# Kernel tuning notes

Measured on AMD Instinct MI355X. Metric: run time of the kernel, lower is better.

The kernel has to match this reference:

```python
import jax, jax.numpy as jnp
import numpy as np

IN_FEATURES = 1024
N_CLASSES = 50257
CUTOFFS = [2000, 10000]      # head covers [0,2000); clusters [2000,10000), [10000,50257)
DIV_VALUE = 4.0
IGNORE_INDEX = -1
N_ROWS = 4096
HEAD_SIZE = CUTOFFS[0] + len(CUTOFFS)  # 2002 (head classes + one slot per tail cluster)
HSZ = [int(IN_FEATURES // (DIV_VALUE ** (i + 1))) for i in range(len(CUTOFFS))]  # [256, 64]
BOUNDS = CUTOFFS + [N_CLASSES]


def setup_inputs() -> dict:
    key = jax.random.key(0)
    ks = jax.random.split(key, 8)
    x = jax.random.normal(ks[0], (N_ROWS, IN_FEATURES), dtype=jnp.float32)
    target = jax.random.randint(ks[1], (N_ROWS,), 0, N_CLASSES, dtype=jnp.int64)
    drop = jax.random.uniform(ks[2], (N_ROWS,)) < 0.1
    target = jnp.where(drop, IGNORE_INDEX, target)
    s = 1.0 / np.sqrt(IN_FEATURES)
    head_w = jax.random.normal(ks[3], (HEAD_SIZE, IN_FEATURES), dtype=jnp.float32) * s
    proj0 = jax.random.normal(ks[4], (HSZ[0], IN_FEATURES), dtype=jnp.float32) * s
    out0 = jax.random.normal(ks[5], (BOUNDS[1] - BOUNDS[0], HSZ[0]), dtype=jnp.float32) * (1.0 / np.sqrt(HSZ[0]))
    proj1 = jax.random.normal(ks[6], (HSZ[1], IN_FEATURES), dtype=jnp.float32) * s
    out1 = jax.random.normal(ks[7], (BOUNDS[2] - BOUNDS[1], HSZ[1]), dtype=jnp.float32) * (1.0 / np.sqrt(HSZ[1]))
    return {"x": x, "target": target, "head_w": head_w,
            "proj0": proj0, "out0": out0, "proj1": proj1, "out1": out1}


def reference(x, target, head_w, proj0, out0, proj1, out1):
    # head: [N, cutoff0 + n_clusters] logits, shared log-softmax
    head_lp = jax.nn.log_softmax(jnp.einsum('nd,hd->nh', x, head_w), axis=-1)
    rows = jnp.arange(x.shape[0])
    valid = target != IGNORE_INDEX
    t = jnp.where(valid, target, 0)

    # head-band targets: log prob directly from head
    t_head = jnp.clip(t, 0, CUTOFFS[0] - 1)
    logp = head_lp[rows, t_head]

    # tail clusters: head cluster-slot logprob + within-cluster logprob
    tails = [(proj0, out0), (proj1, out1)]
    for i, (proj, out) in enumerate(tails):
        low, high = BOUNDS[i], BOUNDS[i + 1]
        # [N, hsz] @ [hsz, osz] -> [N, osz] cluster logits
        cl_lp = jax.nn.log_softmax(
            jnp.einsum('nh,oh->no', jnp.einsum('nd,hd->nh', x, proj), out), axis=-1)
        rel = jnp.clip(t - low, 0, high - low - 1)
        cand = head_lp[:, CUTOFFS[0] + i] + cl_lp[rows, rel]
        logp = jnp.where((t >= low) & (t < high), cand, logp)

    # ignore-index filter + mean == masked mean over valid rows
    vf = valid.astype(logp.dtype)
    loss = -(logp * vf).sum() / vf.sum()
    return loss
```

## Files before the change

kernel.cpp:

```cpp
#include <hip/hip_runtime.h>
#include <hip/hip_bf16.h>

typedef __attribute__((ext_vector_type(8))) short bf16x8;
typedef __attribute__((ext_vector_type(4))) float f32x4;
typedef unsigned short u16;

constexpr int NR      = 4096;
constexpr int INF     = 1024;
constexpr int HEAD_N  = 2002;
constexpr int HEAD_NP = 2048;
constexpr int C0_LO   = 2000, C0_HI = 10000;
constexpr int C0_N    = 8000;
constexpr int C1_N    = 40257;
constexpr int C1_NP   = 40320;
constexpr int K0      = 256;
constexpr int K1      = 64;
constexpr int PCAT    = 320;
constexpr int PCAT_P  = 384;
constexpr int WCAT_R  = HEAD_NP + PCAT_P;
constexpr int IGNORE  = -1;
constexpr float LOG2E = 1.4426950408889634f;
constexpr float LN2   = 0.6931471805599453f;

constexpr int S0      = 16;
constexpr int S1      = 10;
constexpr int NHP     = 32;
constexpr int MEGA_GRID = 1024 + 512;

static __device__ __forceinline__ u16 f32_to_bf16(float f) {
    unsigned int u = __float_as_uint(f);
    return (u16)((u + 0x7FFFu + ((u >> 16) & 1u)) >> 16);
}

static __device__ __forceinline__ float fast_exp2(float x) {
#if __has_builtin(__builtin_amdgcn_exp2f)
    return __builtin_amdgcn_exp2f(x);
#else
    return __expf(x * LN2);
#endif
}

static __device__ __forceinline__ void gload_lds16(const u16* g, u16* l) {
    __builtin_amdgcn_global_load_lds(
        (const __attribute__((address_space(1))) unsigned int*)g,
        (__attribute__((address_space(3))) unsigned int*)l, 16, 0, 0);
}

struct CvtSegs { const float* s[6]; u16* d[6]; int n8[6]; float sc[6]; };

__global__ void cvt_multi(CvtSegs segs) {
    const int stride = gridDim.x * blockDim.x;
    const int gid = blockIdx.x * blockDim.x + threadIdx.x;
#pragma unroll
    for (int seg = 0; seg < 6; ++seg) {
        const float4* sp = (const float4*)segs.s[seg];
        bf16x8* dp = (bf16x8*)segs.d[seg];
        const int n8 = segs.n8[seg];
        const float sc = segs.sc[seg];
        for (int i = gid; i < n8; i += stride) {
            float4 a = sp[2 * i], b = sp[2 * i + 1];
            bf16x8 o;
            o[0] = (short)f32_to_bf16(a.x * sc); o[1] = (short)f32_to_bf16(a.y * sc);
            o[2] = (short)f32_to_bf16(a.z * sc); o[3] = (short)f32_to_bf16(a.w * sc);
            o[4] = (short)f32_to_bf16(b.x * sc); o[5] = (short)f32_to_bf16(b.y * sc);
            o[6] = (short)f32_to_bf16(b.z * sc); o[7] = (short)f32_to_bf16(b.w * sc);
            dp[i] = o;
        }
    }
}

__global__ void compact_kernel(const int* __restrict__ tgt,
                               int* __restrict__ c0list, int* __restrict__ c1list,
                               int* __restrict__ crow, int* __restrict__ cnts) {
    __shared__ int b0, b1;
    if (threadIdx.x == 0) { b0 = 0; b1 = 0; }
    __syncthreads();
#pragma unroll
    for (int i = 0; i < 4; ++i) {
        const int r = threadIdx.x + i * 1024;
        const int t = tgt[r];
        if (t >= C0_LO && t < C0_HI) { int s = atomicAdd(&b0, 1); c0list[s] = r; crow[r] = s; }
        else if (t >= C0_HI)         { int s = atomicAdd(&b1, 1); c1list[s] = r; crow[r] = s; }
        else crow[r] = 0;
    }
    __syncthreads();
    const int c0 = b0, c1 = b1;
    const int p0 = (c0 + 127) & ~127, p1 = (c1 + 127) & ~127;
    if (threadIdx.x == 0) { cnts[0] = c0; cnts[1] = c1; cnts[2] = p0; cnts[3] = p1; }
    for (int i = c0 + (int)threadIdx.x; i < p0; i += 1024) c0list[i] = 0;
    for (int i = c1 + (int)threadIdx.x; i < p1; i += 1024) c1list[i] = 0;
}

__launch_bounds__(256, 2)
__global__ void proj_tile(const u16* __restrict__ A, const u16* __restrict__ B,
                          float* __restrict__ HF, u16* __restrict__ HB)
{
    constexpr int K = INF;
    __shared__ u16 ldsA[128 * 64];
    __shared__ u16 ldsB[128 * 64];
    const int tid = threadIdx.x, wid = tid >> 6, lane = tid & 63;
    const int wr = wid >> 1, wc = wid & 1;
    const int row0 = blockIdx.x * 128, col0 = blockIdx.y * 128;

    f32x4 acc[4][4];
#pragma unroll
    for (int m = 0; m < 4; ++m)
#pragma unroll
        for (int n = 0; n < 4; ++n) acc[m][n] = (f32x4){0.f, 0.f, 0.f, 0.f};

    const int srow = lane >> 3;
    const int ssw  = (lane & 7) ^ srow;

    for (int ks = 0; ks < K / 64; ++ks) {
        const int k0 = ks * 64;
#pragma unroll
        for (int q = 0; q < 4; ++q) {
            const int c = q * 4 + wid, row = c * 8 + srow;
            gload_lds16(A + (size_t)(row0 + row) * K + k0 + ssw * 8, ldsA + c * 512);
        }
#pragma unroll
        for (int q = 0; q < 4; ++q) {
            const int c = q * 4 + wid, row = c * 8 + srow;
            gload_lds16(B + (size_t)(col0 + row) * K + k0 + ssw * 8, ldsB + c * 512);
        }
        __syncthreads();
        const bf16x8* A8 = (const bf16x8*)ldsA;
        const bf16x8* B8 = (const bf16x8*)ldsB;
        bf16x8 af[4][2], bfr[4][2];
#pragma unroll
        for (int m = 0; m < 4; ++m) {
            const int ar = wr * 64 + m * 16 + (lane & 15);
#pragma unroll
            for (int ks2 = 0; ks2 < 2; ++ks2)
                af[m][ks2] = A8[ar * 8 + ((ks2 * 4 + (lane >> 4)) ^ (ar & 7))];
        }
#pragma unroll
        for (int n = 0; n < 4; ++n) {
            const int br = wc * 64 + n * 16 + (lane & 15);
#pragma unroll
            for (int ks2 = 0; ks2 < 2; ++ks2)
                bfr[n][ks2] = B8[br * 8 + ((ks2 * 4 + (lane >> 4)) ^ (br & 7))];
        }
#pragma unroll
        for (int ks2 = 0; ks2 < 2; ++ks2)
#pragma unroll
            for (int m = 0; m < 4; ++m)
#pragma unroll
                for (int n = 0; n < 4; ++n)
                    acc[m][n] = __builtin_amdgcn_mfma_f32_16x16x32_bf16(
                        af[m][ks2], bfr[n][ks2], acc[m][n], 0, 0, 0);
        __syncthreads();
    }
#pragma unroll
    for (int m = 0; m < 4; ++m)
#pragma unroll
        for (int n = 0; n < 4; ++n) {
            const int col = col0 + wc * 64 + n * 16 + (lane & 15);
            if (col < PCAT) {
#pragma unroll
                for (int r = 0; r < 4; ++r) {
                    const int row = row0 + wr * 64 + m * 16 + (lane >> 4) * 4 + r;
                    const float v = acc[m][n][r];
                    HF[(size_t)row * PCAT + col] = v;
                    HB[(size_t)row * PCAT + col] = f32_to_bf16(v);
                }
            }
        }
}

static __device__ void head_section(int rb, int ct,
                                    const u16* __restrict__ A, const u16* __restrict__ B,
                                    const int* __restrict__ tgt,
                                    float* __restrict__ SEHp, float* __restrict__ TL,
                                    u16* ldsA, u16* ldsB, int* sth)
{
    constexpr int K = INF;
    const int tid = threadIdx.x, wid = tid >> 6, lane = tid & 63;
    const int wr = wid >> 1, wc = wid & 1;
    const int row0 = rb * 128, col0 = ct * 128;

    if (tid < 128) {
        int t = tgt[row0 + tid];
        sth[tid] = (t < 0) ? 0 : (t < C0_LO ? t : (t < C0_HI ? C0_LO : C0_LO + 1));
    }

    f32x4 acc[4][4];
#pragma unroll
    for (int m = 0; m < 4; ++m)
#pragma unroll
        for (int n = 0; n < 4; ++n) acc[m][n] = (f32x4){0.f, 0.f, 0.f, 0.f};

    const int srow = lane >> 3;
    const int ssw  = (lane & 7) ^ srow;

    for (int ks = 0; ks < K / 64; ++ks) {
        const int k0 = ks * 64;
#pragma unroll
        for (int q = 0; q < 4; ++q) {
            const int c = q * 4 + wid, row = c * 8 + srow;
            gload_lds16(A + (size_t)(row0 + row) * K + k0 + ssw * 8, ldsA + c * 512);
        }
#pragma unroll
        for (int q = 0; q < 4; ++q) {
            const int c = q * 4 + wid, row = c * 8 + srow;
            gload_lds16(B + (size_t)(col0 + row) * K + k0 + ssw * 8, ldsB + c * 512);
        }
        __syncthreads();
        const bf16x8* A8 = (const bf16x8*)ldsA;
        const bf16x8* B8 = (const bf16x8*)ldsB;
        bf16x8 af[4][2], bfr[4][2];
#pragma unroll
        for (int m = 0; m < 4; ++m) {
            const int ar = wr * 64 + m * 16 + (lane & 15);
#pragma unroll
            for (int ks2 = 0; ks2 < 2; ++ks2)
                af[m][ks2] = A8[ar * 8 + ((ks2 * 4 + (lane >> 4)) ^ (ar & 7))];
        }
#pragma unroll
        for (int n = 0; n < 4; ++n) {
            const int br = wc * 64 + n * 16 + (lane & 15);
#pragma unroll
            for (int ks2 = 0; ks2 < 2; ++ks2)
                bfr[n][ks2] = B8[br * 8 + ((ks2 * 4 + (lane >> 4)) ^ (br & 7))];
        }
#pragma unroll
        for (int ks2 = 0; ks2 < 2; ++ks2)
#pragma unroll
            for (int m = 0; m < 4; ++m)
#pragma unroll
                for (int n = 0; n < 4; ++n)
                    acc[m][n] = __builtin_amdgcn_mfma_f32_16x16x32_bf16(
                        af[m][ks2], bfr[n][ks2], acc[m][n], 0, 0, 0);
        __syncthreads();
    }

    const int slot = ct * 2 + wc;
#pragma unroll
    for (int m = 0; m < 4; ++m) {
        f32x4 rs = (f32x4){0.f, 0.f, 0.f, 0.f};
#pragma unroll
        for (int n = 0; n < 4; ++n) {
            const int cls = col0 + wc * 64 + n * 16 + (lane & 15);
            if (cls < HEAD_N) {
#pragma unroll
                for (int r = 0; r < 4; ++r) {
                    rs[r] += fast_exp2(acc[m][n][r]);
                    const int lrow = wr * 64 + m * 16 + (lane >> 4) * 4 + r;
                    if (sth[lrow] == cls) TL[row0 + lrow] = acc[m][n][r];
                }
            }
        }
#pragma unroll
        for (int msk = 1; msk < 16; msk <<= 1)
#pragma unroll
            for (int r = 0; r < 4; ++r) rs[r] += __shfl_xor(rs[r], msk, 64);
        if ((lane & 15) == 0) {
            const int rbase = row0 + wr * 64 + m * 16 + (lane >> 4) * 4;
#pragma unroll
            for (int r = 0; r < 4; ++r) SEHp[(size_t)slot * NR + rbase + r] = rs[r];
        }
    }
}

template<int K, int CT>
static __device__ void sumexp_section(const u16* __restrict__ Hbase, int ldh,
                                      const int* __restrict__ list,
                                      const u16* __restrict__ W,
                                      int nreal, int ntiles, int tps,
                                      int rb, int split, float* __restrict__ SEp,
                                      u16* lds)
{
    constexpr int MSETS = 2;
    constexpr int NKF   = K / 32;
    constexpr int SLOTS = K / 8;
    constexpr int CHUNKS = CT * K * 2 / 4096;
    constexpr int RPC   = 256 / SLOTS;
    constexpr int NT    = CT / 16;

    const int tid = threadIdx.x, wid = tid >> 6, lane = tid & 63;
    const int row0 = rb * 128 + wid * 32;

    const int t0 = split * tps;
    const int t1 = min(t0 + tps, ntiles);

    bf16x8 afr[MSETS][NKF];
#pragma unroll
    for (int m = 0; m < MSETS; ++m) {
        const int orow = list[row0 + m * 16 + (lane & 15)];
        const u16* hr = Hbase + (size_t)orow * ldh + (lane >> 4) * 8;
#pragma unroll
        for (int kf = 0; kf < NKF; ++kf)
            afr[m][kf] = *(const bf16x8*)(hr + kf * 32);
    }

    float rs[MSETS][4];
#pragma unroll
    for (int m = 0; m < MSETS; ++m)
#pragma unroll
        for (int r = 0; r < 4; ++r) rs[m][r] = 0.f;

    const int trow  = tid / SLOTS;
    const int swoff = ((tid % SLOTS) ^ (trow & 7)) * 8;

    auto STAGE = [&](int t, int buf) {
        const u16* wb = W + (size_t)t * CT * K + (size_t)trow * K + swoff;
        u16* lb = lds + buf * (CT * K) + wid * 512;
#pragma unroll
        for (int c = 0; c < CHUNKS; ++c)
            gload_lds16(wb + (size_t)c * RPC * K, lb + c * 2048);
    };

    int cur = 0;
    STAGE(t0, 0);
    __syncthreads();

    for (int t = t0; t < t1; ++t) {
        if (t + 1 < t1) STAGE(t + 1, cur ^ 1);
        const bf16x8* B8 = (const bf16x8*)(lds + cur * (CT * K));
        const bool full = (t + 1) * CT <= nreal;
#pragma unroll
        for (int n = 0; n < NT; ++n) {
            const int br = n * 16 + (lane & 15);
            bf16x8 bfr[NKF];
#pragma unroll
            for (int kf = 0; kf < NKF; ++kf)
                bfr[kf] = B8[br * SLOTS + ((kf * 4 + (lane >> 4)) ^ (br & 7))];
            f32x4 acc[MSETS];
#pragma unroll
            for (int m = 0; m < MSETS; ++m) acc[m] = (f32x4){0.f, 0.f, 0.f, 0.f};
#pragma unroll
            for (int m = 0; m < MSETS; ++m)
#pragma unroll
                for (int kf = 0; kf < NKF; ++kf)
                    acc[m] = __builtin_amdgcn_mfma_f32_16x16x32_bf16(
                        afr[m][kf], bfr[kf], acc[m], 0, 0, 0);
            if (full || (t * CT + n * 16 + (lane & 15)) < nreal) {
#pragma unroll
                for (int m = 0; m < MSETS; ++m)
#pragma unroll
                    for (int r = 0; r < 4; ++r) rs[m][r] += fast_exp2(acc[m][r]);
            }
        }
        __syncthreads();
        cur ^= 1;
    }

#pragma unroll
    for (int msk = 1; msk < 16; msk <<= 1)
#pragma unroll
        for (int m = 0; m < MSETS; ++m)
#pragma unroll
            for (int r = 0; r < 4; ++r) rs[m][r] += __shfl_xor(rs[m][r], msk, 64);
    if ((lane & 15) == 0) {
        const int rbase = row0 + (lane >> 4) * 4;
#pragma unroll
        for (int m = 0; m < MSETS; ++m)
#pragma unroll
            for (int r = 0; r < 4; ++r)
                SEp[(size_t)split * NR + rbase + m * 16 + r] = rs[m][r];
    }
}

__launch_bounds__(256, 3)
__global__ void mega_kernel(const u16* __restrict__ xb, const u16* __restrict__ wcatb,
                            const u16* __restrict__ hcatb,
                            const u16* __restrict__ o0b, const u16* __restrict__ o1b,
                            const int* __restrict__ tgt,
                            const int* __restrict__ c0list, const int* __restrict__ c1list,
                            const int* __restrict__ cnts,
                            float* __restrict__ SEHp, float* __restrict__ TL,
                            float* __restrict__ C0p, float* __restrict__ C1p)
{
    __shared__ u16 smem[2][8192];
    __shared__ int sth[128];
    const int bid = blockIdx.x;

    if (bid < 1024) {
        if ((bid & 1) == 0) {
            const int h = bid >> 1;
            head_section(h >> 4, h & 15, xb, wcatb, tgt, SEHp, TL,
                         smem[0], smem[1], sth);
        } else {
            const int c = bid >> 1;
            const int rb = c / S1, split = c - rb * S1;
            if (rb * 128 < cnts[3])
                sumexp_section<K1, 128>(hcatb + 256, PCAT, c1list, o1b,
                                        C1_N, C1_NP / 128, 32, rb, split, C1p, smem[0]);
        }
    } else {
        const int idx = bid - 1024;
        const int rb = idx >> 4, split = idx & 15;
        if (rb * 128 < cnts[2])
            sumexp_section<K0, 32>(hcatb, PCAT, c0list, o0b,
                                   C0_N, C0_N / 32, 16, rb, split, C0p, smem[0]);
    }
}

__global__ void epilogue_kernel(const int* __restrict__ tgt, const float* __restrict__ tl,
                                const float* __restrict__ out0, const float* __restrict__ out1,
                                const float* __restrict__ hcatf,
                                const float* __restrict__ SEHp, const float* __restrict__ C0p,
                                const float* __restrict__ C1p, const int* __restrict__ crow,
                                float* __restrict__ rowlogp, float* __restrict__ rowvalid) {
    const int wid = threadIdx.x >> 6, lane = threadIdx.x & 63;
    const int r = blockIdx.x * 4 + wid;
    const int t = tgt[r];
    const bool valid = (t != IGNORE);
    const int tc = valid ? t : 0;
    const int band = (tc < C0_LO) ? 0 : (tc < C0_HI) ? 1 : 2;
    const int cr = crow[r];

    float p2 = 0.f;
    if (band == 1) {
        const float* hr = hcatf + (size_t)r * PCAT;
        const float* crp = out0 + (size_t)(tc - C0_LO) * K0;
        for (int k = lane; k < K0; k += 64) p2 += hr[k] * crp[k];
    } else if (band == 2) {
        p2 = hcatf[(size_t)r * PCAT + 256 + lane] * out1[(size_t)(tc - C0_HI) * K1 + lane];
    }
#pragma unroll
    for (int msk = 32; msk >= 1; msk >>= 1) p2 += __shfl_xor(p2, msk, 64);

    float hp = (lane < NHP) ? SEHp[(size_t)lane * NR + r] : 0.f;
    float cp = 0.f;
    if (band == 1 && lane < S0) cp = C0p[(size_t)lane * NR + cr];
    if (band == 2 && lane < S1) cp = C1p[(size_t)lane * NR + cr];
#pragma unroll
    for (int msk = 1; msk < 32; msk <<= 1) {
        hp += __shfl_xor(hp, msk, 64);
        cp += __shfl_xor(cp, msk, 64);
    }

    if (lane == 0) {
        float logp = LN2 * tl[r] - __logf(hp);
        if (band != 0) logp += p2 - __logf(cp);
        rowlogp[r]  = valid ? logp : 0.f;
        rowvalid[r] = valid ? 1.f : 0.f;
    }
}

__global__ void final_reduce(const float* __restrict__ rowlogp,
                             const float* __restrict__ rowvalid, float* __restrict__ out) {
    __shared__ float sl[256], sv[256];
    const int tid = threadIdx.x;
    float a = 0.f, b = 0.f;
    for (int i = tid; i < NR; i += 256) { a += rowlogp[i]; b += rowvalid[i]; }
    sl[tid] = a; sv[tid] = b;
    __syncthreads();
    for (int s = 128; s > 0; s >>= 1) {
        if (tid < s) { sl[tid] += sl[tid + s]; sv[tid] += sv[tid + s]; }
        __syncthreads();
    }
    if (tid == 0) out[0] = -sl[0] / sv[0];
}

extern "C" void kernel_launch(void* const* d_in, const int* in_sizes, int n_in,
                              void* d_out, int out_size, void* d_ws, size_t ws_size,
                              hipStream_t stream) {
    const float* x      = (const float*)d_in[0];
    const int*   tgt    = (const int*)d_in[1];
    const float* head_w = (const float*)d_in[2];
    const float* proj0  = (const float*)d_in[3];
    const float* out0   = (const float*)d_in[4];
    const float* proj1  = (const float*)d_in[5];
    const float* out1   = (const float*)d_in[6];
    float* loss = (float*)d_out;

    char* base = (char*)d_ws;
    size_t off = 0;
    auto alloc = [&](size_t bytes) { char* p = base + off; off += (bytes + 255) & ~(size_t)255; return p; };

    u16* xb    = (u16*)alloc((size_t)NR * INF * 2);
    u16* wcatb = (u16*)alloc((size_t)WCAT_R * INF * 2);
    u16* o0b   = (u16*)alloc((size_t)C0_N * K0 * 2);
    u16* o1b   = (u16*)alloc((size_t)C1_NP * K1 * 2);
    float* hcatf = (float*)alloc((size_t)NR * PCAT * 4);
    u16*   hcatb = (u16*)alloc((size_t)NR * PCAT * 2);
    float* SEHp = (float*)alloc((size_t)NHP * NR * 4);
    float* C0p  = (float*)alloc((size_t)S0 * NR * 4);
    float* C1p  = (float*)alloc((size_t)S1 * NR * 4);
    float* tl   = (float*)alloc((size_t)NR * 4);
    int* c0list = (int*)alloc((size_t)(NR + 128) * 4);
    int* c1list = (int*)alloc((size_t)(NR + 128) * 4);
    int* crow   = (int*)alloc((size_t)NR * 4);
    int* cnts   = (int*)alloc(4 * 4);
    float* rowlogp  = (float*)alloc((size_t)NR * 4);
    float* rowvalid = (float*)alloc((size_t)NR * 4);

    compact_kernel<<<1, 1024, 0, stream>>>(tgt, c0list, c1list, crow, cnts);

    CvtSegs segs;
    segs.s[0] = x;      segs.d[0] = xb;                              segs.n8[0] = NR * INF / 8;      segs.sc[0] = 1.0f;
    segs.s[1] = head_w; segs.d[1] = wcatb;                           segs.n8[1] = HEAD_N * INF / 8;  segs.sc[1] = LOG2E;
    segs.s[2] = proj0;  segs.d[2] = wcatb + (size_t)HEAD_NP * INF;   segs.n8[2] = 256 * INF / 8;     segs.sc[2] = 1.0f;
    segs.s[3] = proj1;  segs.d[3] = wcatb + (size_t)(HEAD_NP + 256) * INF; segs.n8[3] = 64 * INF / 8; segs.sc[3] = 1.0f;
    segs.s[4] = out0;   segs.d[4] = o0b;                             segs.n8[4] = C0_N * K0 / 8;     segs.sc[4] = LOG2E;
    segs.s[5] = out1;   segs.d[5] = o1b;                             segs.n8[5] = C1_N * K1 / 8;     segs.sc[5] = LOG2E;
    cvt_multi<<<2048, 256, 0, stream>>>(segs);

    proj_tile<<<dim3(32, PCAT_P / 128), 256, 0, stream>>>(xb, wcatb + (size_t)HEAD_NP * INF, hcatf, hcatb);

    mega_kernel<<<MEGA_GRID, 256, 0, stream>>>(xb, wcatb, hcatb, o0b, o1b, tgt,
                                               c0list, c1list, cnts, SEHp, tl, C0p, C1p);

    epilogue_kernel<<<NR / 4, 256, 0, stream>>>(tgt, tl, out0, out1, hcatf,
                                                SEHp, C0p, C1p, crow, rowlogp, rowvalid);
    final_reduce<<<1, 256, 0, stream>>>(rowlogp, rowvalid, loss);
    (void)in_sizes; (void)n_in; (void)out_size; (void)ws_size;
}
```

Baseline: 100.5 us.

## Fuse compaction into convert, re-split cluster sumexp, fuse epilogue with final reduce

Merges the target-compaction kernel into the bf16 conversion kernel (block 0, using wave ballots) and folds the final reduction into the epilogue via atomics plus a last-block-done counter, cutting two launches. It drops the fp32 projection output and makes the epilogue read bf16 hidden states. It also raises cluster sumexp splits (16→50, 10→40) so more blocks share the work and blocks are no longer interleaved with head tiles. This risks small accuracy loss from bf16 hidden values and float atomic ordering nondeterminism. Finer splits add partial-sum traffic.

```diff
diff --git a/kernel.cpp b/kernel.cpp
--- a/kernel.cpp
+++ b/kernel.cpp
@@ -22,14 +22,23 @@
 constexpr float LOG2E = 1.4426950408889634f;
 constexpr float LN2   = 0.6931471805599453f;
 
-constexpr int S0      = 16;
-constexpr int S1      = 10;
+constexpr int S0      = 50;
+constexpr int TPS0    = 5;
+constexpr int S1      = 40;
+constexpr int TPS1    = 8;
 constexpr int NHP     = 32;
-constexpr int MEGA_GRID = 1024 + 512;
+constexpr int HEADB   = 512;
+constexpr int C1B     = 32 * S1;
+constexpr int C0B     = 32 * S0;
+constexpr int MEGA_GRID = HEADB + C1B + C0B;
 
 static __device__ __forceinline__ u16 f32_to_bf16(float f) {
     unsigned int u = __float_as_uint(f);
     return (u16)((u + 0x7FFFu + ((u >> 16) & 1u)) >> 16);
+}
+static __device__ __forceinline__ float bf2f(u16 v) {
+    unsigned int u = ((unsigned int)v) << 16;
+    return __uint_as_float(u);
 }
 
 static __device__ __forceinline__ float fast_exp2(float x) {
@@ -48,7 +57,43 @@
 
 struct CvtSegs { const float* s[6]; u16* d[6]; int n8[6]; float sc[6]; };
 
-__global__ void cvt_multi(CvtSegs segs) {
+__global__ void cvt_compact(CvtSegs segs, const int* __restrict__ tgt,
+                            int* __restrict__ c0list, int* __restrict__ c1list,
+                            int* __restrict__ crow, int* __restrict__ cnts,
+                            float* __restrict__ accum, int* __restrict__ done) {
+    if (blockIdx.x == 0) {
+        __shared__ int b0s, b1s;
+        const int tid = threadIdx.x;
+        const int lane = tid & 63;
+        if (tid == 0) { b0s = 0; b1s = 0; accum[0] = 0.f; accum[1] = 0.f; done[0] = 0; }
+        __syncthreads();
+        for (int it = 0; it < NR / 256; ++it) {
+            const int r = it * 256 + tid;
+            const int t = tgt[r];
+            const bool in0 = (t >= C0_LO) && (t < C0_HI);
+            const bool in1 = (t >= C0_HI);
+            unsigned long long m0 = __ballot(in0);
+            unsigned long long m1 = __ballot(in1);
+            int base0 = 0, base1 = 0;
+            if (lane == 0) {
+                base0 = atomicAdd(&b0s, (int)__popcll(m0));
+                base1 = atomicAdd(&b1s, (int)__popcll(m1));
+            }
+            base0 = __shfl(base0, 0, 64);
+            base1 = __shfl(base1, 0, 64);
+            const unsigned long long lt = (1ULL << lane) - 1ULL;
+            if (in0) { int s = base0 + (int)__popcll(m0 & lt); c0list[s] = r; crow[r] = s; }
+            else if (in1) { int s = base1 + (int)__popcll(m1 & lt); c1list[s] = r; crow[r] = s; }
+            else crow[r] = 0;
+        }
+        __syncthreads();
+        const int c0 = b0s, c1 = b1s;
+        const int p0 = (c0 + 127) & ~127, p1 = (c1 + 127) & ~127;
+        if (threadIdx.x == 0) { cnts[0] = c0; cnts[1] = c1; cnts[2] = p0; cnts[3] = p1; }
+        for (int i = c0 + (int)threadIdx.x; i < p0; i += 256) c0list[i] = 0;
+        for (int i = c1 + (int)threadIdx.x; i < p1; i += 256) c1list[i] = 0;
+    }
+
     const int stride = gridDim.x * blockDim.x;
     const int gid = blockIdx.x * blockDim.x + threadIdx.x;
 #pragma unroll
@@ -69,31 +114,9 @@
     }
 }
 
-__global__ void compact_kernel(const int* __restrict__ tgt,
-                               int* __restrict__ c0list, int* __restrict__ c1list,
-                               int* __restrict__ crow, int* __restrict__ cnts) {
-    __shared__ int b0, b1;
-    if (threadIdx.x == 0) { b0 = 0; b1 = 0; }
-    __syncthreads();
-#pragma unroll
-    for (int i = 0; i < 4; ++i) {
-        const int r = threadIdx.x + i * 1024;
-        const int t = tgt[r];
-        if (t >= C0_LO && t < C0_HI) { int s = atomicAdd(&b0, 1); c0list[s] = r; crow[r] = s; }
-        else if (t >= C0_HI)         { int s = atomicAdd(&b1, 1); c1list[s] = r; crow[r] = s; }
-        else crow[r] = 0;
-    }
-    __syncthreads();
-    const int c0 = b0, c1 = b1;
-    const int p0 = (c0 + 127) & ~127, p1 = (c1 + 127) & ~127;
-    if (threadIdx.x == 0) { cnts[0] = c0; cnts[1] = c1; cnts[2] = p0; cnts[3] = p1; }
-    for (int i = c0 + (int)threadIdx.x; i < p0; i += 1024) c0list[i] = 0;
-    for (int i = c1 + (int)threadIdx.x; i < p1; i += 1024) c1list[i] = 0;
-}
-
 __launch_bounds__(256, 2)
 __global__ void proj_tile(const u16* __restrict__ A, const u16* __restrict__ B,
-                          float* __restrict__ HF, u16* __restrict__ HB)
+                          u16* __restrict__ HB)
 {
     constexpr int K = INF;
     __shared__ u16 ldsA[128 * 64];
@@ -160,9 +183,7 @@
 #pragma unroll
                 for (int r = 0; r < 4; ++r) {
                     const int row = row0 + wr * 64 + m * 16 + (lane >> 4) * 4 + r;
-                    const float v = acc[m][n][r];
-                    HF[(size_t)row * PCAT + col] = v;
-                    HB[(size_t)row * PCAT + col] = f32_to_bf16(v);
+                    HB[(size_t)row * PCAT + col] = f32_to_bf16(acc[m][n][r]);
                 }
             }
         }
@@ -375,33 +396,31 @@
     __shared__ int sth[128];
     const int bid = blockIdx.x;
 
-    if (bid < 1024) {
-        if ((bid & 1) == 0) {
-            const int h = bid >> 1;
-            head_section(h >> 4, h & 15, xb, wcatb, tgt, SEHp, TL,
-                         smem[0], smem[1], sth);
-        } else {
-            const int c = bid >> 1;
-            const int rb = c / S1, split = c - rb * S1;
-            if (rb * 128 < cnts[3])
-                sumexp_section<K1, 128>(hcatb + 256, PCAT, c1list, o1b,
-                                        C1_N, C1_NP / 128, 32, rb, split, C1p, smem[0]);
-        }
+    if (bid < HEADB) {
+        head_section(bid >> 4, bid & 15, xb, wcatb, tgt, SEHp, TL,
+                     smem[0], smem[1], sth);
+    } else if (bid < HEADB + C1B) {
+        const int c = bid - HEADB;
+        const int rb = c / S1, split = c - rb * S1;
+        if (rb * 128 < cnts[3])
+            sumexp_section<K1, 128>(hcatb + 256, PCAT, c1list, o1b,
+                                    C1_N, C1_NP / 128, TPS1, rb, split, C1p, smem[0]);
     } else {
-        const int idx = bid - 1024;
-        const int rb = idx >> 4, split = idx & 15;
+        const int idx = bid - (HEADB + C1B);
+        const int rb = idx / S0, split = idx - rb * S0;
         if (rb * 128 < cnts[2])
             sumexp_section<K0, 32>(hcatb, PCAT, c0list, o0b,
-                                   C0_N, C0_N / 32, 16, rb, split, C0p, smem[0]);
-    }
-}
-
-__global__ void epilogue_kernel(const int* __restrict__ tgt, const float* __restrict__ tl,
-                                const float* __restrict__ out0, const float* __restrict__ out1,
-                                const float* __restrict__ hcatf,
-                                const float* __restrict__ SEHp, const float* __restrict__ C0p,
-                                const float* __restrict__ C1p, const int* __restrict__ crow,
-                                float* __restrict__ rowlogp, float* __restrict__ rowvalid) {
+                                   C0_N, C0_N / 32, TPS0, rb, split, C0p, smem[0]);
+    }
+}
+
+__global__ void epifinal(const int* __restrict__ tgt, const float* __restrict__ tl,
+                         const float* __restrict__ out0, const float* __restrict__ out1,
+                         const u16* __restrict__ hcatb,
+                         const float* __restrict__ SEHp, const float* __restrict__ C0p,
+                         const float* __restrict__ C1p, const int* __restrict__ crow,
+                         float* __restrict__ accum, int* __restrict__ done,
+                         float* __restrict__ loss) {
     const int wid = threadIdx.x >> 6, lane = threadIdx.x & 63;
     const int r = blockIdx.x * 4 + wid;
     const int t = tgt[r];
@@ -412,11 +431,11 @@
 
     float p2 = 0.f;
     if (band == 1) {
-        const float* hr = hcatf + (size_t)r * PCAT;
+        const u16* hr = hcatb + (size_t)r * PCAT;
         const float* crp = out0 + (size_t)(tc - C0_LO) * K0;
-        for (int k = lane; k < K0; k += 64) p2 += hr[k] * crp[k];
+        for (int k = lane; k < K0; k += 64) p2 += bf2f(hr[k]) * crp[k];
     } else if (band == 2) {
-        p2 = hcatf[(size_t)r * PCAT + 256 + lane] * out1[(size_t)(tc - C0_HI) * K1 + lane];
+        p2 = bf2f(hcatb[(size_t)r * PCAT + 256 + lane]) * out1[(size_t)(tc - C0_HI) * K1 + lane];
     }
 #pragma unroll
     for (int msk = 32; msk >= 1; msk >>= 1) p2 += __shfl_xor(p2, msk, 64);
@@ -426,32 +445,30 @@
     if (band == 1 && lane < S0) cp = C0p[(size_t)lane * NR + cr];
     if (band == 2 && lane < S1) cp = C1p[(size_t)lane * NR + cr];
 #pragma unroll
-    for (int msk = 1; msk < 32; msk <<= 1) {
+    for (int msk = 1; msk < 64; msk <<= 1) {
         hp += __shfl_xor(hp, msk, 64);
         cp += __shfl_xor(cp, msk, 64);
     }
 
+    __shared__ float sl[4], sv[4];
     if (lane == 0) {
         float logp = LN2 * tl[r] - __logf(hp);
         if (band != 0) logp += p2 - __logf(cp);
-        rowlogp[r]  = valid ? logp : 0.f;
-        rowvalid[r] = valid ? 1.f : 0.f;
-    }
-}
-
-__global__ void final_reduce(const float* __restrict__ rowlogp,
-                             const float* __restrict__ rowvalid, float* __restrict__ out) {
-    __shared__ float sl[256], sv[256];
-    const int tid = threadIdx.x;
-    float a = 0.f, b = 0.f;
-    for (int i = tid; i < NR; i += 256) { a += rowlogp[i]; b += rowvalid[i]; }
-    sl[tid] = a; sv[tid] = b;
+        sl[wid] = valid ? logp : 0.f;
+        sv[wid] = valid ? 1.f : 0.f;
+    }
     __syncthreads();
-    for (int s = 128; s > 0; s >>= 1) {
-        if (tid < s) { sl[tid] += sl[tid + s]; sv[tid] += sv[tid + s]; }
-        __syncthreads();
-    }
-    if (tid == 0) out[0] = -sl[0] / sv[0];
+    if (threadIdx.x == 0) {
+        atomicAdd(&accum[0], sl[0] + sl[1] + sl[2] + sl[3]);
+        atomicAdd(&accum[1], sv[0] + sv[1] + sv[2] + sv[3]);
+        __threadfence();
+        const int prev = atomicAdd(done, 1);
+        if (prev == (int)gridDim.x - 1) {
+            const float A = atomicAdd(&accum[0], 0.0f);
+            const float B = atomicAdd(&accum[1], 0.0f);
+            loss[0] = -A / B;
+        }
+    }
 }
 
 extern "C" void kernel_launch(void* const* d_in, const int* in_sizes, int n_in,
@@ -474,8 +491,7 @@
     u16* wcatb = (u16*)alloc((size_t)WCAT_R * INF * 2);
     u16* o0b   = (u16*)alloc((size_t)C0_N * K0 * 2);
     u16* o1b   = (u16*)alloc((size_t)C1_NP * K1 * 2);
-    float* hcatf = (float*)alloc((size_t)NR * PCAT * 4);
-    u16*   hcatb = (u16*)alloc((size_t)NR * PCAT * 2);
+    u16* hcatb = (u16*)alloc((size_t)NR * PCAT * 2);
     float* SEHp = (float*)alloc((size_t)NHP * NR * 4);
     float* C0p  = (float*)alloc((size_t)S0 * NR * 4);
     float* C1p  = (float*)alloc((size_t)S1 * NR * 4);
@@ -484,10 +500,8 @@
     int* c1list = (int*)alloc((size_t)(NR + 128) * 4);
     int* crow   = (int*)alloc((size_t)NR * 4);
     int* cnts   = (int*)alloc(4 * 4);
-    float* rowlogp  = (float*)alloc((size_t)NR * 4);
-    float* rowvalid = (float*)alloc((size_t)NR * 4);
-
-    compact_kernel<<<1, 1024, 0, stream>>>(tgt, c0list, c1list, crow, cnts);
+    float* accum = (float*)alloc(2 * 4);
+    int*   done  = (int*)alloc(4);
 
     CvtSegs segs;
     segs.s[0] = x;      segs.d[0] = xb;                              segs.n8[0] = NR * INF / 8;      segs.sc[0] = 1.0f;
@@ -496,15 +510,14 @@
     segs.s[3] = proj1;  segs.d[3] = wcatb + (size_t)(HEAD_NP + 256) * INF; segs.n8[3] = 64 * INF / 8; segs.sc[3] = 1.0f;
     segs.s[4] = out0;   segs.d[4] = o0b;                             segs.n8[4] = C0_N * K0 / 8;     segs.sc[4] = LOG2E;
     segs.s[5] = out1;   segs.d[5] = o1b;                             segs.n8[5] = C1_N * K1 / 8;     segs.sc[5] = LOG2E;
-    cvt_multi<<<2048, 256, 0, stream>>>(segs);
-
-    proj_tile<<<dim3(32, PCAT_P / 128), 256, 0, stream>>>(xb, wcatb + (size_t)HEAD_NP * INF, hcatf, hcatb);
+    cvt_compact<<<2048, 256, 0, stream>>>(segs, tgt, c0list, c1list, crow, cnts, accum, done);
+
+    proj_tile<<<dim3(32, PCAT_P / 128), 256, 0, stream>>>(xb, wcatb + (size_t)HEAD_NP * INF, hcatb);
 
     mega_kernel<<<MEGA_GRID, 256, 0, stream>>>(xb, wcatb, hcatb, o0b, o1b, tgt,
                                                c0list, c1list, cnts, SEHp, tl, C0p, C1p);
 
-    epilogue_kernel<<<NR / 4, 256, 0, stream>>>(tgt, tl, out0, out1, hcatf,
-                                                SEHp, C0p, C1p, crow, rowlogp, rowvalid);
-    final_reduce<<<1, 256, 0, stream>>>(rowlogp, rowvalid, loss);
+    epifinal<<<NR / 4, 256, 0, stream>>>(tgt, tl, out0, out1, hcatb,
+                                         SEHp, C0p, C1p, crow, accum, done, loss);
     (void)in_sizes; (void)n_in; (void)out_size; (void)ws_size;
 }
```

After: 111.4 us. 1.11x slower.
